# Kernel tuning notes

Hardware: AMD Instinct MI355X
Metric: run time of the kernel (lower is better)

## Reference

```python
import math
import jax, jax.numpy as jnp
import numpy as np

DIM = 256; DEPTH = 5; FANOUT = 10; VOCAB = 257
B = 16; T = 2048
NEXP = 8; HID = 512; TOPK = 2; TEMP = 1.0; HEADS = 2
CAPACITY = math.ceil(B * TOPK / NEXP * 1.1)  # capacity-based dispatch, =5
LAYER_SIZES = [FANOUT ** l for l in range(DEPTH)]  # [1,10,100,1000,10000]


def setup_inputs() -> dict:
    key = jax.random.key(0)
    ks = iter(jax.random.split(key, 64))
    def p(shape, scale=0.02):
        return jax.random.normal(next(ks), shape, jnp.float32) * scale
    inp = {
        'tokens': jax.random.randint(next(ks), (B, T), 0, VOCAB),
        'embed': p((VOCAB, DIM)),
        'pin_w': p((DIM, DIM)), 'pin_b': jnp.zeros(DIM, jnp.float32),
        'pch_w': p((DIM, DIM)), 'pch_b': jnp.zeros(DIM, jnp.float32),
        'depth_bias': p((DEPTH, DIM)),
        'q_w': p((DIM, DIM)), 'q_b': jnp.zeros(DIM, jnp.float32),
        'k_w': p((DIM, DIM)), 'k_b': jnp.zeros(DIM, jnp.float32),
        'v_w': p((DIM, DIM)), 'v_b': jnp.zeros(DIM, jnp.float32),
        'o_w': p((DIM, DIM)), 'o_b': jnp.zeros(DIM, jnp.float32),
        'level_gate': jnp.zeros(DEPTH, jnp.float32),
        'depth_gate': jnp.zeros((DEPTH, DIM), jnp.float32),
        'in_proj_w': p((DIM, 3 * DIM)), 'in_proj_b': jnp.zeros(3 * DIM, jnp.float32),
        'out_proj_w': p((DIM, DIM)), 'out_proj_b': jnp.zeros(DIM, jnp.float32),
        'ln_g': jnp.ones(DIM, jnp.float32), 'ln_b': jnp.zeros(DIM, jnp.float32),
        'ic_gate': jnp.zeros(1, jnp.float32),
        'gate_w': p((DIM, NEXP)), 'gate_b': jnp.zeros(NEXP, jnp.float32),
        'ew1': p((NEXP, DIM, HID)), 'eb1': jnp.zeros((NEXP, HID), jnp.float32),
        'ew2': p((NEXP, HID, DIM)), 'eb2': jnp.zeros((NEXP, DIM), jnp.float32),
        'hw1': p((DIM, DIM)), 'hb1': jnp.zeros(DIM, jnp.float32),
        'hw2': p((DIM, VOCAB)), 'hb2': jnp.zeros(VOCAB, jnp.float32),
    }
    return inp


def _fractal(context, pin_w, pin_b, pch_w, pch_b, depth_bias, q_w, q_b, k_w, k_b,
             v_w, v_b, o_w, o_b, level_gate, depth_gate,
             in_proj_w, in_proj_b, out_proj_w, out_proj_b, ln_g, ln_b, ic_gate):
    Bc = context.shape[0]
    base = context @ pin_w + pin_b                       # [B,D]
    y_next = None
    level_means = [None] * DEPTH
    inv_sqrt_d = 1.0 / math.sqrt(DIM)
    for l in reversed(range(DEPTH)):
        n = LAYER_SIZES[l]
        if l == DEPTH - 1:
            child_agg = jnp.zeros((Bc, n, DIM), context.dtype)
        else:
            yg = y_next.reshape(Bc, n, FANOUT, DIM)      # children grouped per parent
            q = (base + depth_bias[l]) @ q_w + q_b       # [B,D], shared across nodes
            k = yg @ k_w + k_b
            v = yg @ v_w + v_b
            att = jax.nn.softmax(jnp.einsum('bd,bnfd->bnf', q, k) * inv_sqrt_d, axis=-1)
            child_agg = jax.nn.sigmoid(depth_gate[l]) * jnp.einsum('bnf,bnfd->bnd', att, v)
        gate = jax.nn.sigmoid(level_gate[l])
        upd = (base[:, None, :] + depth_bias[l][None, None, :] + child_agg @ pch_w + pch_b) * gate
        y = jax.nn.relu(upd) @ o_w + o_b                 # [B,n,D]
        level_means[l] = y.mean(axis=1)
        y_next = y
    root = y_next[:, 0, :]                               # n==1 at level 0
    # interconnect: MHA over per-level means [B,DEPTH,D]
    z = jnp.stack(level_means, axis=1)
    qkv = z @ in_proj_w + in_proj_b
    qh, kh, vh = jnp.split(qkv, 3, axis=-1)
    hd = DIM // HEADS
    def to_heads(t):
        return t.reshape(Bc, DEPTH, HEADS, hd).transpose(0, 2, 1, 3)
    qh, kh, vh = to_heads(qh), to_heads(kh), to_heads(vh)
    aw = jax.nn.softmax(jnp.einsum('bhqd,bhkd->bhqk', qh, kh) / math.sqrt(hd), axis=-1)
    z2 = jnp.einsum('bhqk,bhkd->bhqd', aw, vh).transpose(0, 2, 1, 3).reshape(Bc, DEPTH, DIM)
    z2 = z2 @ out_proj_w + out_proj_b
    zs = z + z2
    mu = zs.mean(-1, keepdims=True)
    var = ((zs - mu) ** 2).mean(-1, keepdims=True)
    zn = (zs - mu) / jnp.sqrt(var + 1e-5) * ln_g + ln_b
    return root + jax.nn.sigmoid(ic_gate) * zn[:, 0, :]


def _moe(ctx, gate_w, gate_b, ew1, eb1, ew2, eb2):
    scaled = (ctx @ gate_w + gate_b) / TEMP
    top_vals, top_idx = jax.lax.top_k(scaled, TOPK)      # [B,K]
    gs = jax.nn.softmax(top_vals, axis=-1)               # [B,K], strictly > 0
    out = jnp.zeros_like(ctx)
    for e in range(NEXP):                                # fixed small expert loop
        sflat = jnp.where(top_idx == e, gs, -1.0).reshape(-1)   # [B*K]
        vals, pos = jax.lax.top_k(sflat, CAPACITY)       # capacity-limited dispatch
        w = jnp.where(vals > 0.0, vals, 0.0)             # drop unassigned/overflow
        tok = pos // TOPK
        xin = ctx[tok]                                   # [cap,D]
        eo = jax.nn.relu(xin @ ew1[e] + eb1[e]) @ ew2[e] + eb2[e]
        out = out.at[tok].add(eo * w[:, None])
    return out


def reference(tokens, embed, pin_w, pin_b, pch_w, pch_b, depth_bias,
              q_w, q_b, k_w, k_b, v_w, v_b, o_w, o_b, level_gate, depth_gate,
              in_proj_w, in_proj_b, out_proj_w, out_proj_b, ln_g, ln_b, ic_gate,
              gate_w, gate_b, ew1, eb1, ew2, eb2, hw1, hb1, hw2, hb2):
    x = embed[tokens]                                    # [B,T,D]
    context = x.mean(axis=1)                             # [B,D]
    root = _fractal(context, pin_w, pin_b, pch_w, pch_b, depth_bias, q_w, q_b,
                    k_w, k_b, v_w, v_b, o_w, o_b, level_gate, depth_gate,
                    in_proj_w, in_proj_b, out_proj_w, out_proj_b, ln_g, ln_b, ic_gate)
    root = root + _moe(root, gate_w, gate_b, ew1, eb1, ew2, eb2)
    h = x + root[:, None, :]                             # per-token logits from context + token emb
    logits = jax.nn.relu(h @ hw1 + hb1) @ hw2 + hb2      # [B,T,V]
    return logits
```

## Files before the change

### kernel.cpp

```cpp
#include <hip/hip_runtime.h>
#include <hip/hip_bf16.h>
#include <math.h>

#define DIM    256
#define DEPTH  5
#define FANOUT 10
#define VOCAB  257
#define BB     16
#define TT     2048
#define NEXP   8
#define HID    512
#define TOPK   2
#define CAP    5

__device__ __forceinline__ float sigm(float x) { return 1.f / (1.f + expf(-x)); }

__device__ __forceinline__ void mv8x2(const float* sv, const float* __restrict__ W,
                                      int kseg, int cq, float red[16][DIM]) {
  const float* Wp = W + (size_t)kseg * 16 * DIM + cq * 4;
  float4 acc = {0.f, 0.f, 0.f, 0.f};
#pragma unroll 1
  for (int h = 0; h < 2; ++h) {
    float4 wv[8];
#pragma unroll
    for (int i = 0; i < 8; ++i)
      wv[i] = *(const float4*)(Wp + (size_t)(h * 8 + i) * DIM);
#pragma unroll
    for (int i = 0; i < 8; ++i) {
      float s = sv[kseg * 16 + h * 8 + i];
      acc.x = fmaf(s, wv[i].x, acc.x);
      acc.y = fmaf(s, wv[i].y, acc.y);
      acc.z = fmaf(s, wv[i].z, acc.z);
      acc.w = fmaf(s, wv[i].w, acc.w);
    }
    __builtin_amdgcn_sched_barrier(0);
  }
  *(float4*)&red[kseg][cq * 4] = acc;
}

__device__ __forceinline__ float sum16(const float red[16][DIM], int d) {
  float s = 0.f;
#pragma unroll
  for (int g = 0; g < 16; ++g) s += red[g][d];
  return s;
}

__global__ void __launch_bounds__(1024) k_fractal(
    const int* __restrict__ tokens, const float* __restrict__ embed,
    const float* __restrict__ pin_w, const float* __restrict__ pin_b,
    const float* __restrict__ pch_w, const float* __restrict__ pch_b,
    const float* __restrict__ depth_bias,
    const float* __restrict__ v_w, const float* __restrict__ v_b,
    const float* __restrict__ o_w, const float* __restrict__ o_b,
    const float* __restrict__ level_gate, const float* __restrict__ depth_gate,
    const float* __restrict__ in_proj_w, const float* __restrict__ in_proj_b,
    const float* __restrict__ out_proj_w, const float* __restrict__ out_proj_b,
    const float* __restrict__ ln_g, const float* __restrict__ ln_b,
    const float* __restrict__ ic_gate,
    float* __restrict__ rootA, float* __restrict__ root2,
    int* __restrict__ bidx, int* __restrict__ boff) {
  int bx = blockIdx.x;
  int tid = threadIdx.x;
  int xcd = bx & 7, slot = bx >> 3;
  __shared__ int cnt[VOCAB];
  __shared__ float sv[DIM];
  __shared__ float basev[DIM];
  __shared__ float ym[DEPTH][DIM];
  __shared__ float q0v[DIM], kh[DEPTH][DIM], vh[DEPTH][DIM];
  __shared__ float red11[4][11][DIM];
  __shared__ float zsv[DIM];
  __shared__ float aw[16];
  __shared__ float redl[8];
  __shared__ int offb[VOCAB + 1];
  __shared__ int woff[VOCAB];
  float (*red16)[DIM] = reinterpret_cast<float(*)[DIM]>(&red11[0][0][0]);

  if (xcd == 1) {
    if (slot < BB) {
      int b = slot;
      for (int i = tid; i < VOCAB; i += 1024) cnt[i] = 0;
      __syncthreads();
      for (int t = tid; t < TT; t += 1024) atomicAdd(&cnt[tokens[b * TT + t]], 1);
      __syncthreads();
      if (tid == 0) {
        int a = 0;
        for (int v = 0; v < VOCAB; ++v) { offb[v] = a; a += cnt[v]; }
        offb[VOCAB] = a;
      }
      __syncthreads();
      if (tid <= VOCAB) boff[b * (VOCAB + 1) + tid] = offb[tid];
      if (tid < VOCAB) woff[tid] = offb[tid];
      __syncthreads();
      for (int t = tid; t < TT; t += 1024) {
        int tok = tokens[b * TT + t];
        int p = atomicAdd(&woff[tok], 1);
        bidx[b * TT + p] = t;
      }
    }
    return;
  }
  if (xcd != 0) return;
  if (slot >= BB) {
    int w = slot - BB;
    float sx = 0.f, sy = 0.f, sz = 0.f, sw = 0.f;
#pragma unroll 1
    for (int q = 0; q < 3; ++q) {
      int r = w * 3 + q;
      if (r >= 37) break;
      const float* W; int n = 16384;
      if (r < 4)       W = pin_w      + (size_t)r * 16384;
      else if (r < 8)  W = pch_w      + (size_t)(r - 4) * 16384;
      else if (r < 12) W = v_w        + (size_t)(r - 8) * 16384;
      else if (r < 16) W = o_w        + (size_t)(r - 12) * 16384;
      else if (r < 20) W = out_proj_w + (size_t)(r - 16) * 16384;
      else if (r < 32) W = in_proj_w  + (size_t)(r - 20) * 16384;
      else { W = embed + (size_t)(r - 32) * 16384; n = 65792 - (r - 32) * 16384;
             if (n > 16384) n = 16384; }
      const float4* src = (const float4*)W + tid;
#pragma unroll
      for (int k = 0; k < 4; ++k) {
        int p = tid * 4 + k * 4096;
        if (p + 4 <= n) {
          float4 v = src[k * 1024];
          sx += v.x; sy += v.y; sz += v.z; sw += v.w;
        }
      }
    }
    asm volatile("" :: "v"(sx), "v"(sy), "v"(sz), "v"(sw));
    return;
  }

  int b = slot;
  int d = tid & 255;
  int ks = tid >> 8;
  int k0 = ks * 64;
  int kseg = tid >> 6;
  int cq = tid & 63;

  for (int i = tid; i < VOCAB; i += 1024) cnt[i] = 0;
  __syncthreads();
  for (int t = tid; t < TT; t += 1024) atomicAdd(&cnt[tokens[b * TT + t]], 1);
  __syncthreads();
  {
    const float* Ep = embed + (size_t)kseg * 16 * DIM + cq * 4;
    float4 acc = {0.f, 0.f, 0.f, 0.f};
#pragma unroll 1
    for (int h = 0; h < 2; ++h) {
      float4 ev[8];
#pragma unroll
      for (int i = 0; i < 8; ++i)
        ev[i] = *(const float4*)(Ep + (size_t)(h * 8 + i) * DIM);
#pragma unroll
      for (int i = 0; i < 8; ++i) {
        float cv = (float)cnt[kseg * 16 + h * 8 + i];
        acc.x = fmaf(cv, ev[i].x, acc.x);
        acc.y = fmaf(cv, ev[i].y, acc.y);
        acc.z = fmaf(cv, ev[i].z, acc.z);
        acc.w = fmaf(cv, ev[i].w, acc.w);
      }
      __builtin_amdgcn_sched_barrier(0);
    }
    *(float4*)&red16[kseg][cq * 4] = acc;
  }
  __syncthreads();
  if (ks == 0) {
    float s = sum16(red16, d);
    s = fmaf((float)cnt[256], embed[(size_t)256 * DIM + d], s);
    sv[d] = s * (1.0f / (float)TT);
  }
  __syncthreads();

  mv8x2(sv, pin_w, kseg, cq, red16);
  __syncthreads();
  if (ks == 0) {
    float base = sum16(red16, d) + pin_b[d];
    basev[d] = base;
    float u = (base + depth_bias[4 * DIM + d] + pch_b[d]) * sigm(level_gate[4]);
    sv[d] = fmaxf(u, 0.f);
  }
  __syncthreads();
  mv8x2(sv, o_w, kseg, cq, red16);
  __syncthreads();
  if (ks == 0) {
    float y = sum16(red16, d) + o_b[d];
    ym[4][d] = y;
    sv[d] = y;
  }
  __syncthreads();
  for (int l = 3; l >= 0; --l) {
    mv8x2(sv, v_w, kseg, cq, red16);
    __syncthreads();
    if (ks == 0) {
      float vv = sum16(red16, d) + v_b[d];
      sv[d] = sigm(depth_gate[l * DIM + d]) * vv;
    }
    __syncthreads();
    mv8x2(sv, pch_w, kseg, cq, red16);
    __syncthreads();
    if (ks == 0) {
      float t = sum16(red16, d) + pch_b[d];
      float u = (basev[d] + depth_bias[l * DIM + d] + t) * sigm(level_gate[l]);
      sv[d] = fmaxf(u, 0.f);
    }
    __syncthreads();
    mv8x2(sv, o_w, kseg, cq, red16);
    __syncthreads();
    if (ks == 0) {
      float y = sum16(red16, d) + o_b[d];
      ym[l][d] = y;
      sv[d] = y;
    }
    __syncthreads();
  }
  {
    float aq = 0.f;
    float ak0 = 0.f, ak1 = 0.f, ak2 = 0.f, ak3 = 0.f, ak4 = 0.f;
    float av0 = 0.f, av1 = 0.f, av2 = 0.f, av3 = 0.f, av4 = 0.f;
#pragma unroll
    for (int h = 0; h < 8; ++h) {
      int kb = k0 + h * 8;
      float wq[8], wk[8], wv8[8];
#pragma unroll
      for (int i = 0; i < 8; ++i) {
        const float* wrow = in_proj_w + (size_t)(kb + i) * 768;
        wq[i] = wrow[d]; wk[i] = wrow[256 + d]; wv8[i] = wrow[512 + d];
      }
#pragma unroll
      for (int i = 0; i < 8; ++i) {
        float z0 = ym[0][kb + i];
        aq  = fmaf(z0, wq[i], aq);
        ak0 = fmaf(z0, wk[i], ak0);
        av0 = fmaf(z0, wv8[i], av0);
        float z1 = ym[1][kb + i];
        ak1 = fmaf(z1, wk[i], ak1);
        av1 = fmaf(z1, wv8[i], av1);
        float z2 = ym[2][kb + i];
        ak2 = fmaf(z2, wk[i], ak2);
        av2 = fmaf(z2, wv8[i], av2);
        float z3 = ym[3][kb + i];
        ak3 = fmaf(z3, wk[i], ak3);
        av3 = fmaf(z3, wv8[i], av3);
        float z4 = ym[4][kb + i];
        ak4 = fmaf(z4, wk[i], ak4);
        av4 = fmaf(z4, wv8[i], av4);
      }
    }
    red11[ks][0][d] = ak0; red11[ks][1][d] = ak1; red11[ks][2][d] = ak2;
    red11[ks][3][d] = ak3; red11[ks][4][d] = ak4;
    red11[ks][5][d] = av0; red11[ks][6][d] = av1; red11[ks][7][d] = av2;
    red11[ks][8][d] = av3; red11[ks][9][d] = av4;
    red11[ks][10][d] = aq;
  }
  __syncthreads();
  for (int idx = tid; idx < 11 * DIM; idx += 1024) {
    int c = idx >> 8, dd = idx & 255;
    float sum = red11[0][c][dd] + red11[1][c][dd] + red11[2][c][dd] + red11[3][c][dd];
    if (c < 5)       kh[c][dd]     = sum + in_proj_b[256 + dd];
    else if (c < 10) vh[c - 5][dd] = sum + in_proj_b[512 + dd];
    else             q0v[dd]       = sum + in_proj_b[dd];
  }
  __syncthreads();
  {
    int wid = tid >> 6;
    if (wid < 10) {
      int h = wid / 5, l = wid - h * 5;
      int lane = tid & 63;
      float s = q0v[h * 128 + lane] * kh[l][h * 128 + lane];
      s = fmaf(q0v[h * 128 + 64 + lane], kh[l][h * 128 + 64 + lane], s);
      for (int o = 32; o > 0; o >>= 1) s += __shfl_down(s, o, 64);
      if (lane == 0) aw[wid] = s * 0.08838834764831845f;
    }
  }
  __syncthreads();
  if (tid < 2) {
    float m = aw[tid * 5];
    for (int l = 1; l < 5; ++l) m = fmaxf(m, aw[tid * 5 + l]);
    float e[5], ssum = 0.f;
    for (int l = 0; l < 5; ++l) { e[l] = expf(aw[tid * 5 + l] - m); ssum += e[l]; }
    for (int l = 0; l < 5; ++l) aw[tid * 5 + l] = e[l] / ssum;
  }
  __syncthreads();
  if (ks == 0) {
    int h = d >> 7;
    float z2 = 0.f;
    for (int l = 0; l < 5; ++l) z2 = fmaf(aw[h * 5 + l], vh[l][d], z2);
    sv[d] = z2;
  }
  __syncthreads();
  mv8x2(sv, out_proj_w, kseg, cq, red16);
  __syncthreads();
  if (ks == 0) {
    float z2p = sum16(red16, d) + out_proj_b[d];
    zsv[d] = ym[0][d] + z2p;
  }
  __syncthreads();
  float zs = 0.f, df = 0.f, mu = 0.f;
  if (tid < 256) {
    zs = zsv[tid];
    float v = zs;
    for (int o = 32; o > 0; o >>= 1) v += __shfl_down(v, o, 64);
    if ((tid & 63) == 0) redl[tid >> 6] = v;
  }
  __syncthreads();
  if (tid < 256) {
    mu = (redl[0] + redl[1] + redl[2] + redl[3]) * (1.f / 256.f);
    df = zs - mu;
  }
  __syncthreads();
  if (tid < 256) {
    float v = df * df;
    for (int o = 32; o > 0; o >>= 1) v += __shfl_down(v, o, 64);
    if ((tid & 63) == 0) redl[tid >> 6] = v;
  }
  __syncthreads();
  if (tid < 256) {
    float var = (redl[0] + redl[1] + redl[2] + redl[3]) * (1.f / 256.f);
    float zn = df / sqrtf(var + 1e-5f) * ln_g[tid] + ln_b[tid];
    float r = ym[0][tid] + sigm(ic_gate[0]) * zn;
    rootA[b * DIM + tid] = r;
    root2[b * DIM + tid] = r;
  }
}

__global__ void __launch_bounds__(256) k_moe(
    const float* __restrict__ rootA,
    const float* __restrict__ gate_w, const float* __restrict__ gate_b,
    const float* __restrict__ ew1, const float* __restrict__ eb1,
    const float* __restrict__ ew2, const float* __restrict__ eb2,
    float* __restrict__ root2) {
  int bx = blockIdx.x;
  int tid = threadIdx.x;
  if (bx >= 64) {
    int r = (bx - 64) % 128;
    const float* W = (r < 64) ? ew1 + (size_t)r * 16384
                              : ew2 + (size_t)(r - 64) * 16384;
    const float4* src = (const float4*)W + tid;
    float sx = 0.f, sy = 0.f, sz = 0.f, sw = 0.f;
#pragma unroll 8
    for (int i = 0; i < 16; ++i) {
      float4 v = src[i * 256];
      sx += v.x; sy += v.y; sz += v.z; sw += v.w;
    }
    asm volatile("" :: "v"(sx), "v"(sy), "v"(sz), "v"(sw));
    return;
  }
  int e = bx >> 3, jt = bx & 7, j0 = jt * 64;
  int w = tid >> 6, lane = tid & 63;
  __shared__ float rlds[BB * DIM];
  __shared__ float gwlds[DIM * NEXP];
  __shared__ float xin[CAP][DIM];
  __shared__ float red[CAP][4][64];
  __shared__ float hloc[CAP][64];
  __shared__ float sc[BB * NEXP];
  __shared__ float gs[BB * TOPK];
  __shared__ int gidx[BB * TOPK];
  __shared__ int stok[CAP];
  __shared__ float swt[CAP];
  for (int idx = tid; idx < BB * DIM / 4; idx += 256)
    *(float4*)&rlds[idx * 4] = *(const float4*)&rootA[idx * 4];
  for (int idx = tid; idx < DIM * NEXP / 4; idx += 256)
    *(float4*)&gwlds[idx * 4] = *(const float4*)&gate_w[idx * 4];
  __syncthreads();
  if (tid < BB * NEXP) {
    int b = tid >> 3, ep = tid & 7;
    float chunk[8];
#pragma unroll
    for (int g = 0; g < 8; ++g) {
      float acc = 0.f;
#pragma unroll 8
      for (int i = 0; i < 32; ++i) {
        int k = g * 32 + i;
        acc = fmaf(rlds[b * DIM + k], gwlds[k * NEXP + ep], acc);
      }
      chunk[g] = acc;
    }
    float s = gate_b[ep];
#pragma unroll
    for (int g = 0; g < 8; ++g) s += chunk[g];
    sc[tid] = s;
  }
  __syncthreads();
  if (tid < BB) {
    int bb = tid;
    int i0 = 0; float v0 = sc[bb * 8 + 0];
    for (int ee = 1; ee < 8; ++ee) { float v = sc[bb * 8 + ee]; if (v > v0) { v0 = v; i0 = ee; } }
    int i1 = -1; float v1 = -1e30f;
    for (int ee = 0; ee < 8; ++ee) {
      if (ee == i0) continue;
      float v = sc[bb * 8 + ee];
      if (v > v1) { v1 = v; i1 = ee; }
    }
    float e1v = expf(v1 - v0);
    float s = 1.f + e1v;
    gs[bb * 2 + 0] = 1.f / s;  gidx[bb * 2 + 0] = i0;
    gs[bb * 2 + 1] = e1v / s;  gidx[bb * 2 + 1] = i1;
  }
  __syncthreads();
  if (tid == 0) {
    unsigned used = 0u;
    for (int s = 0; s < CAP; ++s) {
      int bi = 0; float bv = -1e30f;
      for (int i = 0; i < 32; ++i) {
        if (used & (1u << i)) continue;
        float v = (gidx[i] == e) ? gs[i] : -1.0f;
        if (v > bv) { bv = v; bi = i; }
      }
      used |= (1u << bi);
      stok[s] = bi >> 1;
      swt[s] = bv > 0.f ? bv : 0.f;
    }
  }
  __syncthreads();
  for (int idx = tid; idx < CAP * DIM; idx += 256) {
    int s = idx >> 8, k = idx & 255;
    xin[s][k] = rlds[stok[s] * DIM + k];
  }
  __syncthreads();
  {
    float a0 = 0.f, a1 = 0.f, a2 = 0.f, a3 = 0.f, a4 = 0.f;
    const float* W = ew1 + (size_t)e * DIM * HID + j0 + lane;
    int kbase = w * 64;
#pragma unroll
    for (int h = 0; h < 8; ++h) {
      float wv[8];
#pragma unroll
      for (int i = 0; i < 8; ++i) wv[i] = W[(size_t)(kbase + h * 8 + i) * HID];
#pragma unroll
      for (int i = 0; i < 8; ++i) {
        int k = kbase + h * 8 + i;
        a0 = fmaf(xin[0][k], wv[i], a0);
        a1 = fmaf(xin[1][k], wv[i], a1);
        a2 = fmaf(xin[2][k], wv[i], a2);
        a3 = fmaf(xin[3][k], wv[i], a3);
        a4 = fmaf(xin[4][k], wv[i], a4);
      }
    }
    red[0][w][lane] = a0; red[1][w][lane] = a1; red[2][w][lane] = a2;
    red[3][w][lane] = a3; red[4][w][lane] = a4;
  }
  __syncthreads();
  for (int idx = tid; idx < CAP * 64; idx += 256) {
    int s = idx >> 6, j = idx & 63;
    float sum = red[s][0][j] + red[s][1][j] + red[s][2][j] + red[s][3][j]
              + eb1[e * HID + j0 + j];
    hloc[s][j] = fmaxf(sum, 0.f);
  }
  __syncthreads();
  {
    int d = tid;
    float a0 = 0.f, a1 = 0.f, a2 = 0.f, a3 = 0.f, a4 = 0.f;
    const float* W2 = ew2 + (size_t)e * HID * DIM + (size_t)j0 * DIM + d;
#pragma unroll
    for (int h = 0; h < 8; ++h) {
      float wv[8];
#pragma unroll
      for (int i = 0; i < 8; ++i) wv[i] = W2[(size_t)(h * 8 + i) * DIM];
#pragma unroll
      for (int i = 0; i < 8; ++i) {
        int j = h * 8 + i;
        a0 = fmaf(hloc[0][j], wv[i], a0);
        a1 = fmaf(hloc[1][j], wv[i], a1);
        a2 = fmaf(hloc[2][j], wv[i], a2);
        a3 = fmaf(hloc[3][j], wv[i], a3);
        a4 = fmaf(hloc[4][j], wv[i], a4);
      }
    }
    float bias = (jt == 0) ? eb2[e * DIM + d] : 0.f;
#pragma unroll
    for (int s = 0; s < CAP; ++s) {
      float as = (s == 0) ? a0 : (s == 1) ? a1 : (s == 2) ? a2 : (s == 3) ? a3 : a4;
      float wgt = swt[s];
      if (wgt > 0.f)
        atomicAdd(&root2[stok[s] * DIM + d], (as + bias) * wgt);
    }
  }
}

__global__ void __launch_bounds__(256) k_logits(
    const float* __restrict__ embed, const float* __restrict__ root2,
    const float* __restrict__ hw1, const float* __restrict__ hb1,
    const float* __restrict__ hw2, const float* __restrict__ hb2,
    const int* __restrict__ bidx, const int* __restrict__ boff,
    float* __restrict__ out) {
  int tok = blockIdx.x, r0 = blockIdx.y * 4;
  int c = threadIdx.x;
  __shared__ float hrow[4][DIM];
  __shared__ float hid[4][DIM];
  __shared__ float tailred[4][17];
  __shared__ float tailv[4];
  {
    float ev = embed[(size_t)tok * DIM + c];
#pragma unroll
    for (int j = 0; j < 4; ++j) hrow[j][c] = ev + root2[(size_t)(r0 + j) * DIM + c];
  }
  __syncthreads();
  {
    float a0 = hb1[c], a1 = a0, a2 = a0, a3 = a0;
    for (int kb = 0; kb < DIM; kb += 8) {
      float wv[8];
#pragma unroll
      for (int i = 0; i < 8; ++i) wv[i] = hw1[(size_t)(kb + i) * DIM + c];
#pragma unroll
      for (int i = 0; i < 8; ++i) {
        int k = kb + i;
        a0 = fmaf(hrow[0][k], wv[i], a0);
        a1 = fmaf(hrow[1][k], wv[i], a1);
        a2 = fmaf(hrow[2][k], wv[i], a2);
        a3 = fmaf(hrow[3][k], wv[i], a3);
      }
    }
    hid[0][c] = fmaxf(a0, 0.f); hid[1][c] = fmaxf(a1, 0.f);
    hid[2][c] = fmaxf(a2, 0.f); hid[3][c] = fmaxf(a3, 0.f);
  }
  __syncthreads();
  float a0, a1, a2, a3;
  {
    a0 = hb2[c]; a1 = a0; a2 = a0; a3 = a0;
    for (int kb = 0; kb < DIM; kb += 8) {
      float wv[8];
#pragma unroll
      for (int i = 0; i < 8; ++i) wv[i] = hw2[(size_t)(kb + i) * VOCAB + c];
#pragma unroll
      for (int i = 0; i < 8; ++i) {
        int k = kb + i;
        a0 = fmaf(hid[0][k], wv[i], a0);
        a1 = fmaf(hid[1][k], wv[i], a1);
        a2 = fmaf(hid[2][k], wv[i], a2);
        a3 = fmaf(hid[3][k], wv[i], a3);
      }
    }
  }
  if (c < 64) {
    int r = c >> 4, seg = c & 15;
    float sum = 0.f;
#pragma unroll 4
    for (int i = 0; i < 16; ++i) {
      int k = seg * 16 + i;
      sum = fmaf(hid[r][k], hw2[(size_t)k * VOCAB + 256], sum);
    }
    tailred[r][seg] = sum;
  }
  __syncthreads();
  if (c < 4) {
    float a = hb2[256];
#pragma unroll
    for (int s = 0; s < 16; ++s) a += tailred[c][s];
    tailv[c] = a;
  }
  __syncthreads();
#pragma unroll
  for (int j = 0; j < 4; ++j) {
    int b = r0 + j;
    int s = boff[b * (VOCAB + 1) + tok];
    int e = boff[b * (VOCAB + 1) + tok + 1];
    float aj = (j == 0) ? a0 : (j == 1) ? a1 : (j == 2) ? a2 : a3;
    float tl = tailv[j];
    for (int m = s; m < e; ++m) {
      int t = bidx[b * TT + m];
      size_t base = (size_t)(b * TT + t) * VOCAB;
      out[base + c] = aj;
      if (c == 0) out[base + 256] = tl;
    }
  }
}

extern "C" void kernel_launch(void* const* d_in, const int* in_sizes, int n_in,
                              void* d_out, int out_size, void* d_ws, size_t ws_size,
                              hipStream_t stream) {
  (void)in_sizes; (void)n_in; (void)out_size; (void)ws_size;
  const int*   tokens     = (const int*)d_in[0];
  const float* embed      = (const float*)d_in[1];
  const float* pin_w      = (const float*)d_in[2];
  const float* pin_b      = (const float*)d_in[3];
  const float* pch_w      = (const float*)d_in[4];
  const float* pch_b      = (const float*)d_in[5];
  const float* depth_bias = (const float*)d_in[6];
  const float* v_w        = (const float*)d_in[11];
  const float* v_b        = (const float*)d_in[12];
  const float* o_w        = (const float*)d_in[13];
  const float* o_b        = (const float*)d_in[14];
  const float* level_gate = (const float*)d_in[15];
  const float* depth_gate = (const float*)d_in[16];
  const float* in_proj_w  = (const float*)d_in[17];
  const float* in_proj_b  = (const float*)d_in[18];
  const float* out_proj_w = (const float*)d_in[19];
  const float* out_proj_b = (const float*)d_in[20];
  const float* ln_g       = (const float*)d_in[21];
  const float* ln_b       = (const float*)d_in[22];
  const float* ic_gate    = (const float*)d_in[23];
  const float* gate_w     = (const float*)d_in[24];
  const float* gate_b     = (const float*)d_in[25];
  const float* ew1        = (const float*)d_in[26];
  const float* eb1        = (const float*)d_in[27];
  const float* ew2        = (const float*)d_in[28];
  const float* eb2        = (const float*)d_in[29];
  const float* hw1        = (const float*)d_in[30];
  const float* hb1        = (const float*)d_in[31];
  const float* hw2        = (const float*)d_in[32];
  const float* hb2        = (const float*)d_in[33];
  float* out = (float*)d_out;

  float* ws      = (float*)d_ws;
  float* rootA   = ws + 4096;
  float* root2   = ws + 8192;
  int*   bidx    = (int*)(ws + 43136);
  int*   boff    = (int*)(ws + 75904);

  k_fractal<<<256, 1024, 0, stream>>>(tokens, embed, pin_w, pin_b, pch_w, pch_b,
                                      depth_bias, v_w, v_b, o_w, o_b, level_gate,
                                      depth_gate, in_proj_w, in_proj_b, out_proj_w,
                                      out_proj_b, ln_g, ln_b, ic_gate, rootA, root2,
                                      bidx, boff);
  k_moe<<<256, 256, 0, stream>>>(rootA, gate_w, gate_b, ew1, eb1,
                                 ew2, eb2, root2);
  k_logits<<<dim3(VOCAB, 4), 256, 0, stream>>>(embed, root2, hw1, hb1, hw2, hb2,
                                               bidx, boff, out);
}
```

Baseline: 229.7 us.

## Halve barriers in fractal matvec chain via redundant per-wave reduction and shuffles

The serial chain of 256x256 matvecs now has each wave redundantly reduce the 16 partial sums it needs and broadcast the input vector through wave shuffles, instead of a ks==0 reduction step followed by an extra barrier. Double-buffered partial-sum storage allows one barrier per matvec instead of two. Biases, sigmoid gates and the last embedding row are preloaded into shared memory. In exchange every wave repeats the reduction, adding extra LDS reads and a larger shared-memory footprint.

```diff
diff --git a/kernel.cpp b/kernel.cpp
--- a/kernel.cpp
+++ b/kernel.cpp
@@ -42,6 +42,36 @@
   float s = 0.f;
 #pragma unroll
   for (int g = 0; g < 16; ++g) s += red[g][d];
+  return s;
+}
+
+__device__ __forceinline__ void mvw(float rv, const float* __restrict__ W,
+                                    int kseg, int cq, float* buf) {
+  const float* Wp = W + (size_t)kseg * 16 * DIM + cq * 4;
+  float4 acc = {0.f, 0.f, 0.f, 0.f};
+#pragma unroll 1
+  for (int h = 0; h < 2; ++h) {
+    float4 wv[8];
+#pragma unroll
+    for (int i = 0; i < 8; ++i)
+      wv[i] = *(const float4*)(Wp + (size_t)(h * 8 + i) * DIM);
+#pragma unroll
+    for (int i = 0; i < 8; ++i) {
+      float s = __shfl(rv, h * 8 + i, 64);
+      acc.x = fmaf(s, wv[i].x, acc.x);
+      acc.y = fmaf(s, wv[i].y, acc.y);
+      acc.z = fmaf(s, wv[i].z, acc.z);
+      acc.w = fmaf(s, wv[i].w, acc.w);
+    }
+    __builtin_amdgcn_sched_barrier(0);
+  }
+  *(float4*)&buf[kseg * DIM + cq * 4] = acc;
+}
+
+__device__ __forceinline__ float redw(const float* buf, int dme) {
+  float s = 0.f;
+#pragma unroll
+  for (int g = 0; g < 16; ++g) s += buf[g * DIM + dme];
   return s;
 }
 
@@ -64,7 +94,6 @@
   int xcd = bx & 7, slot = bx >> 3;
   __shared__ int cnt[VOCAB];
   __shared__ float sv[DIM];
-  __shared__ float basev[DIM];
   __shared__ float ym[DEPTH][DIM];
   __shared__ float q0v[DIM], kh[DEPTH][DIM], vh[DEPTH][DIM];
   __shared__ float red11[4][11][DIM];
@@ -73,7 +102,11 @@
   __shared__ float redl[8];
   __shared__ int offb[VOCAB + 1];
   __shared__ int woff[VOCAB];
+  __shared__ float pre[14][DIM];
+  __shared__ float lg_s[DEPTH];
   float (*red16)[DIM] = reinterpret_cast<float(*)[DIM]>(&red11[0][0][0]);
+  float* bufA = &red11[0][0][0];
+  float* bufB = bufA + 4096;
 
   if (xcd == 1) {
     if (slot < BB) {
@@ -136,8 +169,18 @@
   int k0 = ks * 64;
   int kseg = tid >> 6;
   int cq = tid & 63;
+  int lane = tid & 63;
+  int dme = kseg * 16 + (lane & 15);
 
   for (int i = tid; i < VOCAB; i += 1024) cnt[i] = 0;
+  for (int i = tid; i < DIM; i += 1024) {
+    pre[0][i] = pin_b[i]; pre[1][i] = o_b[i];
+    pre[2][i] = pch_b[i]; pre[3][i] = v_b[i];
+    pre[13][i] = embed[(size_t)256 * DIM + i];
+  }
+  for (int i = tid; i < 5 * DIM; i += 1024) pre[4 + (i >> 8)][i & 255] = depth_bias[i];
+  for (int i = tid; i < 4 * DIM; i += 1024) pre[9 + (i >> 8)][i & 255] = sigm(depth_gate[i]);
+  if (tid < DEPTH) lg_s[tid] = sigm(level_gate[tid]);
   __syncthreads();
   for (int t = tid; t < TT; t += 1024) atomicAdd(&cnt[tokens[b * TT + t]], 1);
   __syncthreads();
@@ -160,58 +203,56 @@
       }
       __builtin_amdgcn_sched_barrier(0);
     }
-    *(float4*)&red16[kseg][cq * 4] = acc;
-  }
-  __syncthreads();
-  if (ks == 0) {
-    float s = sum16(red16, d);
-    s = fmaf((float)cnt[256], embed[(size_t)256 * DIM + d], s);
-    sv[d] = s * (1.0f / (float)TT);
-  }
-  __syncthreads();
-
-  mv8x2(sv, pin_w, kseg, cq, red16);
-  __syncthreads();
-  if (ks == 0) {
-    float base = sum16(red16, d) + pin_b[d];
-    basev[d] = base;
-    float u = (base + depth_bias[4 * DIM + d] + pch_b[d]) * sigm(level_gate[4]);
-    sv[d] = fmaxf(u, 0.f);
-  }
-  __syncthreads();
-  mv8x2(sv, o_w, kseg, cq, red16);
-  __syncthreads();
-  if (ks == 0) {
-    float y = sum16(red16, d) + o_b[d];
-    ym[4][d] = y;
-    sv[d] = y;
-  }
-  __syncthreads();
+    *(float4*)&bufA[kseg * DIM + cq * 4] = acc;
+  }
+  __syncthreads();
+  float* cur = bufB; float* prv = bufA;
+  float rv, base_r;
+  {
+    float s = redw(prv, dme);
+    s = fmaf((float)cnt[256], pre[13][dme], s);
+    rv = s * (1.0f / (float)TT);
+  }
+  mvw(rv, pin_w, kseg, cq, cur);
+  __syncthreads();
+  { float* t = cur; cur = prv; prv = t; }
+  {
+    base_r = redw(prv, dme) + pre[0][dme];
+    float u = (base_r + pre[8][dme] + pre[2][dme]) * lg_s[4];
+    rv = fmaxf(u, 0.f);
+  }
+  mvw(rv, o_w, kseg, cq, cur);
+  __syncthreads();
+  { float* t = cur; cur = prv; prv = t; }
+  {
+    float y = redw(prv, dme) + pre[1][dme];
+    if (lane < 16) ym[4][dme] = y;
+    rv = y;
+  }
+#pragma unroll 1
   for (int l = 3; l >= 0; --l) {
-    mv8x2(sv, v_w, kseg, cq, red16);
+    mvw(rv, v_w, kseg, cq, cur);
     __syncthreads();
-    if (ks == 0) {
-      float vv = sum16(red16, d) + v_b[d];
-      sv[d] = sigm(depth_gate[l * DIM + d]) * vv;
-    }
+    { float* t = cur; cur = prv; prv = t; }
+    rv = pre[9 + l][dme] * (redw(prv, dme) + pre[3][dme]);
+    mvw(rv, pch_w, kseg, cq, cur);
     __syncthreads();
-    mv8x2(sv, pch_w, kseg, cq, red16);
+    { float* t = cur; cur = prv; prv = t; }
+    {
+      float t2 = redw(prv, dme) + pre[2][dme];
+      float u = (base_r + pre[4 + l][dme] + t2) * lg_s[l];
+      rv = fmaxf(u, 0.f);
+    }
+    mvw(rv, o_w, kseg, cq, cur);
     __syncthreads();
-    if (ks == 0) {
-      float t = sum16(red16, d) + pch_b[d];
-      float u = (basev[d] + depth_bias[l * DIM + d] + t) * sigm(level_gate[l]);
-      sv[d] = fmaxf(u, 0.f);
-    }
-    __syncthreads();
-    mv8x2(sv, o_w, kseg, cq, red16);
-    __syncthreads();
-    if (ks == 0) {
-      float y = sum16(red16, d) + o_b[d];
-      ym[l][d] = y;
-      sv[d] = y;
-    }
-    __syncthreads();
-  }
+    { float* t = cur; cur = prv; prv = t; }
+    {
+      float y = redw(prv, dme) + pre[1][dme];
+      if (lane < 16) ym[l][dme] = y;
+      rv = y;
+    }
+  }
+  __syncthreads();
   {
     float aq = 0.f;
     float ak0 = 0.f, ak1 = 0.f, ak2 = 0.f, ak3 = 0.f, ak4 = 0.f;
@@ -264,11 +305,11 @@
     int wid = tid >> 6;
     if (wid < 10) {
       int h = wid / 5, l = wid - h * 5;
-      int lane = tid & 63;
-      float s = q0v[h * 128 + lane] * kh[l][h * 128 + lane];
-      s = fmaf(q0v[h * 128 + 64 + lane], kh[l][h * 128 + 64 + lane], s);
+      int ln2 = tid & 63;
+      float s = q0v[h * 128 + ln2] * kh[l][h * 128 + ln2];
+      s = fmaf(q0v[h * 128 + 64 + ln2], kh[l][h * 128 + 64 + ln2], s);
       for (int o = 32; o > 0; o >>= 1) s += __shfl_down(s, o, 64);
-      if (lane == 0) aw[wid] = s * 0.08838834764831845f;
+      if (ln2 == 0) aw[wid] = s * 0.08838834764831845f;
     }
   }
   __syncthreads();
```

Measured after the change: 229.6 us. No clear change (-0.0%).
